# Kernel tuning notes

Measured on AMD Instinct MI355X. Metric: run time of the kernel, lower is better.

## Reference

```python
import jax, jax.numpy as jnp
import numpy as np

N_HEAD = 16
ROPE_BASE = 10000.0
ROPE_SCALE = 1.0

B, T, C = 4, 2048, 1024


def _rope_cos_sin(seq_len, head_dim, dtype):
    inv_freq = 1.0 / (ROPE_BASE ** (jnp.arange(0, head_dim, 2, dtype=jnp.float32) / head_dim))
    t = jnp.arange(seq_len, dtype=jnp.float32) * ROPE_SCALE
    freqs = jnp.einsum('t,d->td', t, inv_freq)          # [T, D/2]
    emb = jnp.concatenate([freqs, freqs], axis=-1)       # [T, D]
    return jnp.cos(emb).astype(dtype), jnp.sin(emb).astype(dtype)


def _rotate_half(x):
    x1, x2 = jnp.split(x, 2, axis=-1)
    return jnp.concatenate([-x2, x1], axis=-1)


def setup_inputs() -> dict:
    key = jax.random.key(0)
    ks = jax.random.split(key, 5)
    s = 1.0 / np.sqrt(C)  # modest init scale to keep logits sane
    return {
        'x': jax.random.normal(ks[0], (B, T, C), dtype=jnp.float32),
        'wq': jax.random.normal(ks[1], (C, C), dtype=jnp.float32) * s,
        'wk': jax.random.normal(ks[2], (C, C), dtype=jnp.float32) * s,
        'wv': jax.random.normal(ks[3], (C, C), dtype=jnp.float32) * s,
        'wp': jax.random.normal(ks[4], (C, C), dtype=jnp.float32) * s,
    }


def reference(x, wq, wk, wv, wp):
    # x: [B, T, C]; weights are torch Linear layout [out, in] -> y = x @ W.T
    Bx, Tx, Cx = x.shape
    H = N_HEAD
    D = Cx // H
    scale = D ** -0.5

    def split_heads(y):  # [B,T,C] -> [B,H,T,D]
        return y.reshape(Bx, Tx, H, D).transpose(0, 2, 1, 3)

    q = split_heads(x @ wq.T)
    k = split_heads(x @ wk.T)
    v = split_heads(x @ wv.T)

    cos, sin = _rope_cos_sin(Tx, D, x.dtype)  # [T, D] each
    cos = cos[None, None, :, :]
    sin = sin[None, None, :, :]
    q = q * cos + _rotate_half(q) * sin
    k = k * cos + _rotate_half(k) * sin

    att = jnp.einsum('bhtd,bhsd->bhts', q, k) * scale  # [B,H,T,T]
    causal = jnp.tril(jnp.ones((Tx, Tx), dtype=bool))
    att = jnp.where(causal[None, None], att, -jnp.inf)
    att = jax.nn.softmax(att, axis=-1)

    y = jnp.einsum('bhts,bhsd->bhtd', att, v)          # [B,H,T,D]
    y = y.transpose(0, 2, 1, 3).reshape(Bx, Tx, Cx)    # [B,T,C]
    return y @ wp.T
```

## Files before the change

### kernel.cpp

```cpp
#include <hip/hip_runtime.h>
#include <hip/hip_bf16.h>

typedef __attribute__((ext_vector_type(8))) short short8;
typedef __attribute__((ext_vector_type(4))) float f32x4;
typedef unsigned short u16;

#define DEV static __device__ __forceinline__

constexpr int Bsz = 4, Tn = 2048, Cn = 1024, Hn = 16, Dn = 64;
constexpr int TP = Tn + 32;
constexpr int VROWS = 80;
#define QSCL 0.1803368801111204f

DEV u16 f2bf(float f) {
    union { float f; unsigned u; } v{f};
    return (u16)((v.u + 0x8000u) >> 16);
}
DEV float bf2f(u16 u) {
    union { unsigned u; float f; } v;
    v.u = ((unsigned)u) << 16;
    return v.f;
}

DEV void gload_lds16(const void* g, void* l) {
    __builtin_amdgcn_global_load_lds((const __attribute__((address_space(1))) void*)g,
                                     (__attribute__((address_space(3))) void*)l, 16, 0, 0);
}

__global__ void cvt_kernel(const float* __restrict__ in, u16* __restrict__ out, int n4) {
    int i = blockIdx.x * blockDim.x + threadIdx.x;
    int stride = gridDim.x * blockDim.x;
    for (; i < n4; i += stride) {
        float4 v = ((const float4*)in)[i];
        short4 o;
        o.x = (short)f2bf(v.x); o.y = (short)f2bf(v.y);
        o.z = (short)f2bf(v.z); o.w = (short)f2bf(v.w);
        ((short4*)out)[i] = o;
    }
}

__global__ void cvtw_kernel(const float* __restrict__ w0, const float* __restrict__ w1,
                            const float* __restrict__ w2, const float* __restrict__ w3,
                            u16* o0, u16* o1, u16* o2, u16* o3) {
    const float* src = blockIdx.y == 0 ? w0 : blockIdx.y == 1 ? w1 : blockIdx.y == 2 ? w2 : w3;
    u16* dst = blockIdx.y == 0 ? o0 : blockIdx.y == 1 ? o1 : blockIdx.y == 2 ? o2 : o3;
    int i = blockIdx.x * blockDim.x + threadIdx.x;
    float4 v = ((const float4*)src)[i];
    short4 o;
    o.x = (short)f2bf(v.x); o.y = (short)f2bf(v.y);
    o.z = (short)f2bf(v.z); o.w = (short)f2bf(v.w);
    ((short4*)dst)[i] = o;
}

__global__ void trig_kernel(float* __restrict__ cs, float* __restrict__ sn) {
    int idx = blockIdx.x * blockDim.x + threadIdx.x;
    int t = idx >> 5, i = idx & 31;
    double inv = pow(10000.0, -(double)i / 32.0);
    double a = (double)t * inv;
    cs[idx] = (float)cos(a);
    sn[idx] = (float)sin(a);
}

__global__ void rope_kernel(u16* __restrict__ q, u16* __restrict__ k,
                            const float* __restrict__ cs, const float* __restrict__ sn) {
    int idx = blockIdx.x * blockDim.x + threadIdx.x;
    const int half = Bsz * Hn * Tn * 32;
    float scl = 1.0f;
    u16* p;
    if (idx >= half) { idx -= half; p = k; }
    else             { p = q; scl = QSCL; }
    int row = idx >> 5, i = idx & 31;
    int t = row & (Tn - 1);
    float c = cs[(t << 5) + i], s = sn[(t << 5) + i];
    u16* pr = p + ((long)row << 6);
    float x1 = bf2f(pr[i]), x2 = bf2f(pr[i + 32]);
    pr[i]      = f2bf((x1 * c - x2 * s) * scl);
    pr[i + 32] = f2bf((x2 * c + x1 * s) * scl);
}

__global__ __launch_bounds__(256, 2) void transpose_v(const u16* __restrict__ in,
                                                      u16* __restrict__ out) {
    __shared__ u16 tile[64][68];
    int bh = blockIdx.y;
    long t0 = (long)blockIdx.x * 64;
    int tid = threadIdx.x;
#pragma unroll
    for (int c = 0; c < 2; c++) {
        int idx = c * 256 + tid;
        int r = idx >> 3, col = (idx & 7) << 3;
        *(short8*)&tile[r][col] = *(const short8*)&in[((long)bh * Tn + t0 + r) * 64 + col];
    }
    __syncthreads();
#pragma unroll
    for (int c = 0; c < 2; c++) {
        int idx = c * 256 + tid;
        int d = idx >> 3, tcol = (idx & 7) << 3;
        short8 v;
#pragma unroll
        for (int j = 0; j < 8; j++) v[j] = tile[tcol + j][d];
        *(short8*)&out[((long)bh * VROWS + d) * TP + t0 + tcol] = v;
    }
}

__global__ void fill_ones(u16* __restrict__ vt) {
    long idx = (long)blockIdx.x * 256 + threadIdx.x;
    long bh = idx / (16 * TP);
    long rem = idx % (16 * TP);
    long r = rem / TP, t = rem % TP;
    vt[(bh * VROWS + 64 + r) * TP + t] = (r == 0) ? (u16)0x3f80 : (u16)0;
}

template <int MODE>
__global__ __launch_bounds__(256, 2) void gemm_bt(
    const u16* __restrict__ A,
    const u16* __restrict__ B0, const u16* __restrict__ B1, const u16* __restrict__ B2,
    void* __restrict__ O0, void* __restrict__ O1, void* __restrict__ O2,
    int M, int N, int K) {
    __shared__ u16 As[128 * 32];
    __shared__ u16 Bs[128 * 32];

    const u16* Bp = B0;
    void* Op = O0;
    if (MODE == 0) {
        if (blockIdx.z == 1) { Bp = B1; Op = O1; }
        else if (blockIdx.z == 2) { Bp = B2; Op = O2; }
    }
    int tid = threadIdx.x;
    int w = tid >> 6, lane = tid & 63;
    int lr = lane & 15, lg = lane >> 4;
    int wr = w >> 1, wc = w & 1;
    long brow = (long)blockIdx.x * 128, bcol = (long)blockIdx.y * 128;

    f32x4 acc[4][4] = {};
    const u16* Arow = A + brow * K;
    const u16* Brow = Bp + bcol * K;

    for (int k0 = 0; k0 < K; k0 += 32) {
        __syncthreads();
#pragma unroll
        for (int c = 0; c < 2; c++) {
            int idx = c * 256 + tid;
            int row = idx >> 2, col = (idx & 3) << 3;
            const u16* ga = Arow + (long)row * K + k0 + col;
            const u16* gb = Brow + (long)row * K + k0 + col;
            char* la = (char*)As + (size_t)(c * 256 + (tid & 192)) * 16;
            char* lb = (char*)Bs + (size_t)(c * 256 + (tid & 192)) * 16;
            gload_lds16(ga, la);
            gload_lds16(gb, lb);
        }
        __syncthreads();
        short8 a[4], b[4];
#pragma unroll
        for (int i = 0; i < 4; i++)
            a[i] = *(const short8*)&As[(64 * wr + 16 * i + lr) * 32 + lg * 8];
#pragma unroll
        for (int j = 0; j < 4; j++)
            b[j] = *(const short8*)&Bs[(64 * wc + 16 * j + lr) * 32 + lg * 8];
#pragma unroll
        for (int i = 0; i < 4; i++)
#pragma unroll
            for (int j = 0; j < 4; j++)
                acc[i][j] = __builtin_amdgcn_mfma_f32_16x16x32_bf16(a[i], b[j], acc[i][j], 0, 0, 0);
    }

#pragma unroll
    for (int i = 0; i < 4; i++)
#pragma unroll
        for (int j = 0; j < 4; j++)
#pragma unroll
            for (int jj = 0; jj < 4; jj++) {
                long gr = brow + 64 * wr + 16 * i + lg * 4 + jj;
                long gc = bcol + 64 * wc + 16 * j + lr;
                float v = acc[i][j][jj];
                if (MODE == 0) {
                    long b_ = gr >> 11, t_ = gr & 2047, h_ = gc >> 6, d_ = gc & 63;
                    ((u16*)Op)[(((b_ * Hn + h_) * Tn + t_) << 6) + d_] = f2bf(v);
                } else {
                    ((float*)Op)[gr * N + gc] = v;
                }
            }
}

__global__ __launch_bounds__(256, 2) void attn_kernel(
    const u16* __restrict__ Q, const u16* __restrict__ K, const u16* __restrict__ VT,
    u16* __restrict__ Yb) {
    __shared__ u16 plds[4][32][68];

    int tid = threadIdx.x;
    int w = tid >> 6, lane = tid & 63;
    int lr = lane & 15, lg = lane >> 4;
    int gid = blockIdx.x;
    int xcd = gid & 7;
    int sl = gid >> 3;
    int bh = ((sl >> 3) << 3) + xcd;
    int pairi = (sl & 7) * 4 + w;

    const u16* Qp = Q + (long)bh * Tn * Dn;
    const u16* Kp = K + (long)bh * Tn * Dn;
    const u16* VTp = VT + (long)bh * VROWS * TP;
    long b_ = bh >> 4, h_ = bh & 15;

#pragma unroll
    for (int pass = 0; pass < 2; pass++) {
        int qt = pass == 0 ? pairi : 63 - pairi;
        int q0 = qt * 32;

        short8 aq[2][2];
#pragma unroll
        for (int qi = 0; qi < 2; qi++)
#pragma unroll
            for (int ks = 0; ks < 2; ks++)
                aq[qi][ks] = *(const short8*)&Qp[(long)(q0 + qi * 16 + lr) * 64 + ks * 32 + lg * 8];

        f32x4 acc[2][5] = {};
        float m_[2][4];
#pragma unroll
        for (int qi = 0; qi < 2; qi++)
#pragma unroll
            for (int jj = 0; jj < 4; jj++) m_[qi][jj] = -1e30f;

        auto iter = [&](auto mc, int kv0) {
            constexpr bool MASKED = decltype(mc)::value;
            short8 bk[4][2];
#pragma unroll
            for (int cblk = 0; cblk < 4; cblk++) {
                const u16* kb = &Kp[(long)(kv0 + cblk * 16 + lr) * 64 + lg * 8];
                bk[cblk][0] = *(const short8*)kb;
                bk[cblk][1] = *(const short8*)(kb + 32);
            }
            short8 bv[2][5];
#pragma unroll
            for (int ks = 0; ks < 2; ks++)
#pragma unroll
                for (int dblk = 0; dblk < 5; dblk++)
                    bv[ks][dblk] = *(const short8*)&VTp[(long)(dblk * 16 + lr) * TP + kv0 + ks * 32 + lg * 8];
            f32x4 s[2][4];
#pragma unroll
            for (int cblk = 0; cblk < 4; cblk++)
#pragma unroll
                for (int qi = 0; qi < 2; qi++) {
                    f32x4 sc = {};
                    sc = __builtin_amdgcn_mfma_f32_16x16x32_bf16(aq[qi][0], bk[cblk][0], sc, 0, 0, 0);
                    sc = __builtin_amdgcn_mfma_f32_16x16x32_bf16(aq[qi][1], bk[cblk][1], sc, 0, 0, 0);
                    if (MASKED) {
                        int col = kv0 + cblk * 16 + lr;
#pragma unroll
                        for (int jj = 0; jj < 4; jj++) {
                            int row = q0 + qi * 16 + lg * 4 + jj;
                            if (col > row) sc[jj] = -1e30f;
                        }
                    }
                    s[qi][cblk] = sc;
                }
            float pm[2][4];
            bool grow = false;
#pragma unroll
            for (int qi = 0; qi < 2; qi++)
#pragma unroll
                for (int jj = 0; jj < 4; jj++) {
                    pm[qi][jj] = fmaxf(fmaxf(s[qi][0][jj], s[qi][1][jj]),
                                       fmaxf(s[qi][2][jj], s[qi][3][jj]));
                    grow = grow || (pm[qi][jj] > m_[qi][jj] + 8.0f);
                }
            if (__any(grow)) {
#pragma unroll
                for (int qi = 0; qi < 2; qi++)
#pragma unroll
                    for (int jj = 0; jj < 4; jj++) {
                        float v = pm[qi][jj];
                        v = fmaxf(v, __shfl_xor(v, 1));
                        v = fmaxf(v, __shfl_xor(v, 2));
                        v = fmaxf(v, __shfl_xor(v, 4));
                        v = fmaxf(v, __shfl_xor(v, 8));
                        float mn = fmaxf(m_[qi][jj], v);
                        float alpha = __builtin_amdgcn_exp2f(m_[qi][jj] - mn);
                        m_[qi][jj] = mn;
#pragma unroll
                        for (int dblk = 0; dblk < 5; dblk++) acc[qi][dblk][jj] *= alpha;
                    }
            }
#pragma unroll
            for (int qi = 0; qi < 2; qi++)
#pragma unroll
                for (int cblk = 0; cblk < 4; cblk++)
#pragma unroll
                    for (int jj = 0; jj < 4; jj++)
                        plds[w][qi * 16 + lg * 4 + jj][cblk * 16 + lr] =
                            f2bf(__builtin_amdgcn_exp2f(s[qi][cblk][jj] - m_[qi][jj]));
            short8 pa[2][2];
#pragma unroll
            for (int qi = 0; qi < 2; qi++)
#pragma unroll
                for (int ks = 0; ks < 2; ks++)
                    pa[qi][ks] = *(const short8*)&plds[w][qi * 16 + lr][ks * 32 + lg * 8];
#pragma unroll
            for (int ks = 0; ks < 2; ks++)
#pragma unroll
                for (int dblk = 0; dblk < 5; dblk++)
#pragma unroll
                    for (int qi = 0; qi < 2; qi++)
                        acc[qi][dblk] = __builtin_amdgcn_mfma_f32_16x16x32_bf16(
                            pa[qi][ks], bv[ks][dblk], acc[qi][dblk], 0, 0, 0);
        };

        int kv_end = q0 + 32;
        int last = ((kv_end - 1) >> 6) << 6;
        for (int kv0 = 0; kv0 < last; kv0 += 64)
            iter(std::integral_constant<bool, false>{}, kv0);
        iter(std::integral_constant<bool, true>{}, last);

#pragma unroll
        for (int qi = 0; qi < 2; qi++)
#pragma unroll
            for (int jj = 0; jj < 4; jj++) {
                float l = __shfl(acc[qi][4][jj], lane & 48);
                float rl = 1.0f / l;
                int row = q0 + qi * 16 + lg * 4 + jj;
#pragma unroll
                for (int dblk = 0; dblk < 4; dblk++) {
                    int d = dblk * 16 + lr;
                    Yb[((b_ * Tn + row) * Cn) + h_ * 64 + d] = f2bf(acc[qi][dblk][jj] * rl);
                }
            }
    }
}

extern "C" void kernel_launch(void* const* d_in, const int* in_sizes, int n_in,
                              void* d_out, int out_size, void* d_ws, size_t ws_size,
                              hipStream_t stream) {
    const float* x  = (const float*)d_in[0];
    const float* wq = (const float*)d_in[1];
    const float* wk = (const float*)d_in[2];
    const float* wv = (const float*)d_in[3];
    const float* wp = (const float*)d_in[4];

    char* ws = (char*)d_ws;
    size_t off = 0;
    auto alloc = [&](size_t bytes) {
        char* p = ws + off;
        off += (bytes + 255) & ~(size_t)255;
        return p;
    };
    const size_t BTC = (size_t)Bsz * Tn * Cn;
    u16* xb  = (u16*)alloc(BTC * 2);
    u16* wqb = (u16*)alloc((size_t)Cn * Cn * 2);
    u16* wkb = (u16*)alloc((size_t)Cn * Cn * 2);
    u16* wvb = (u16*)alloc((size_t)Cn * Cn * 2);
    u16* wpb = (u16*)alloc((size_t)Cn * Cn * 2);
    u16* qr  = (u16*)alloc(BTC * 2);
    u16* kr  = (u16*)alloc(BTC * 2);
    u16* vr  = (u16*)alloc(BTC * 2);
    u16* yb  = (u16*)alloc(BTC * 2);
    float* cs = (float*)alloc((size_t)Tn * 32 * 4);
    float* sn = (float*)alloc((size_t)Tn * 32 * 4);
    u16* vt  = xb;

    int M = Bsz * Tn;
    cvt_kernel<<<1024, 256, 0, stream>>>(x, xb, (int)(BTC / 4));
    cvtw_kernel<<<dim3(Cn * Cn / 4 / 256, 4), 256, 0, stream>>>(
        wq, wk, wv, wp, wqb, wkb, wvb, wpb);
    trig_kernel<<<(Tn * 32) / 256, 256, 0, stream>>>(cs, sn);

    gemm_bt<0><<<dim3(M / 128, Cn / 128, 3), 256, 0, stream>>>(
        xb, wqb, wkb, wvb, qr, kr, vr, M, Cn, Cn);

    int nrows = Bsz * Hn * Tn;
    rope_kernel<<<(2 * nrows * 32) / 256, 256, 0, stream>>>(qr, kr, cs, sn);

    transpose_v<<<dim3(Tn / 64, Bsz * Hn), 256, 0, stream>>>(vr, vt);
    fill_ones<<<(64 * 16 * TP) / 256, 256, 0, stream>>>(vt);

    attn_kernel<<<dim3(512), 256, 0, stream>>>(qr, kr, vt, yb);

    gemm_bt<1><<<dim3(M / 128, Cn / 128, 1), 256, 0, stream>>>(
        yb, wpb, wpb, wpb, d_out, nullptr, nullptr, M, Cn, Cn);
}
```

Before: 233.4 us.

## Fuse RoPE into QK GEMM epilogue, write V transposed, widen attention blocks

The QK projection GEMM now applies rotary embedding and the Q scale in its epilogue, pairing accumulator columns d and d+32, so the separate rope kernel goes away. V is computed as W_v·x^T by a new GEMM mode that writes straight into the transposed, padded VT layout, which removes the transpose kernel and the intermediate V buffer. The attention kernel runs 512-thread blocks where each of 8 waves handles one query tile, replacing the two sequential passes per wave. The fused epilogues use scattered 2-byte stores, and the larger attention blocks may change occupancy.

```diff
diff --git a/kernel.cpp b/kernel.cpp
--- a/kernel.cpp
+++ b/kernel.cpp
@@ -61,47 +61,6 @@
     sn[idx] = (float)sin(a);
 }
 
-__global__ void rope_kernel(u16* __restrict__ q, u16* __restrict__ k,
-                            const float* __restrict__ cs, const float* __restrict__ sn) {
-    int idx = blockIdx.x * blockDim.x + threadIdx.x;
-    const int half = Bsz * Hn * Tn * 32;
-    float scl = 1.0f;
-    u16* p;
-    if (idx >= half) { idx -= half; p = k; }
-    else             { p = q; scl = QSCL; }
-    int row = idx >> 5, i = idx & 31;
-    int t = row & (Tn - 1);
-    float c = cs[(t << 5) + i], s = sn[(t << 5) + i];
-    u16* pr = p + ((long)row << 6);
-    float x1 = bf2f(pr[i]), x2 = bf2f(pr[i + 32]);
-    pr[i]      = f2bf((x1 * c - x2 * s) * scl);
-    pr[i + 32] = f2bf((x2 * c + x1 * s) * scl);
-}
-
-__global__ __launch_bounds__(256, 2) void transpose_v(const u16* __restrict__ in,
-                                                      u16* __restrict__ out) {
-    __shared__ u16 tile[64][68];
-    int bh = blockIdx.y;
-    long t0 = (long)blockIdx.x * 64;
-    int tid = threadIdx.x;
-#pragma unroll
-    for (int c = 0; c < 2; c++) {
-        int idx = c * 256 + tid;
-        int r = idx >> 3, col = (idx & 7) << 3;
-        *(short8*)&tile[r][col] = *(const short8*)&in[((long)bh * Tn + t0 + r) * 64 + col];
-    }
-    __syncthreads();
-#pragma unroll
-    for (int c = 0; c < 2; c++) {
-        int idx = c * 256 + tid;
-        int d = idx >> 3, tcol = (idx & 7) << 3;
-        short8 v;
-#pragma unroll
-        for (int j = 0; j < 8; j++) v[j] = tile[tcol + j][d];
-        *(short8*)&out[((long)bh * VROWS + d) * TP + t0 + tcol] = v;
-    }
-}
-
 __global__ void fill_ones(u16* __restrict__ vt) {
     long idx = (long)blockIdx.x * 256 + threadIdx.x;
     long bh = idx / (16 * TP);
@@ -113,17 +72,19 @@
 template <int MODE>
 __global__ __launch_bounds__(256, 2) void gemm_bt(
     const u16* __restrict__ A,
-    const u16* __restrict__ B0, const u16* __restrict__ B1, const u16* __restrict__ B2,
-    void* __restrict__ O0, void* __restrict__ O1, void* __restrict__ O2,
+    const u16* __restrict__ B0, const u16* __restrict__ B1,
+    void* __restrict__ O0, void* __restrict__ O1,
+    const float* __restrict__ CS, const float* __restrict__ SN,
     int M, int N, int K) {
     __shared__ u16 As[128 * 32];
     __shared__ u16 Bs[128 * 32];
 
     const u16* Bp = B0;
     void* Op = O0;
+    float scl = 1.0f;
     if (MODE == 0) {
         if (blockIdx.z == 1) { Bp = B1; Op = O1; }
-        else if (blockIdx.z == 2) { Bp = B2; Op = O2; }
+        else scl = QSCL;
     }
     int tid = threadIdx.x;
     int w = tid >> 6, lane = tid & 63;
@@ -163,28 +124,52 @@
                 acc[i][j] = __builtin_amdgcn_mfma_f32_16x16x32_bf16(a[i], b[j], acc[i][j], 0, 0, 0);
     }
 
-#pragma unroll
-    for (int i = 0; i < 4; i++)
-#pragma unroll
-        for (int j = 0; j < 4; j++)
+    if (MODE == 0) {
+        u16* Op16 = (u16*)Op;
+#pragma unroll
+        for (int i = 0; i < 4; i++)
 #pragma unroll
             for (int jj = 0; jj < 4; jj++) {
                 long gr = brow + 64 * wr + 16 * i + lg * 4 + jj;
-                long gc = bcol + 64 * wc + 16 * j + lr;
-                float v = acc[i][j][jj];
-                if (MODE == 0) {
-                    long b_ = gr >> 11, t_ = gr & 2047, h_ = gc >> 6, d_ = gc & 63;
-                    ((u16*)Op)[(((b_ * Hn + h_) * Tn + t_) << 6) + d_] = f2bf(v);
-                } else {
-                    ((float*)Op)[gr * N + gc] = v;
+                long b_ = gr >> 11, t_ = gr & 2047;
+#pragma unroll
+                for (int j = 0; j < 2; j++) {
+                    int di = 16 * j + lr;
+                    float c = CS[(t_ << 5) + di], s = SN[(t_ << 5) + di];
+                    float x1 = acc[i][j][jj], x2 = acc[i][j + 2][jj];
+                    float o1 = (x1 * c - x2 * s) * scl;
+                    float o2 = (x2 * c + x1 * s) * scl;
+                    long gc = bcol + 64 * wc + 16 * j + lr;
+                    long h_ = gc >> 6;
+                    long base = (((b_ * Hn + h_) * Tn + t_) << 6) + (gc & 63);
+                    Op16[base] = f2bf(o1);
+                    Op16[base + 32] = f2bf(o2);
                 }
             }
-}
-
-__global__ __launch_bounds__(256, 2) void attn_kernel(
+    } else {
+#pragma unroll
+        for (int i = 0; i < 4; i++)
+#pragma unroll
+            for (int j = 0; j < 4; j++)
+#pragma unroll
+                for (int jj = 0; jj < 4; jj++) {
+                    long gr = brow + 64 * wr + 16 * i + lg * 4 + jj;
+                    long gc = bcol + 64 * wc + 16 * j + lr;
+                    float v = acc[i][j][jj];
+                    if (MODE == 1) {
+                        ((float*)Op)[gr * N + gc] = v;
+                    } else {
+                        long h_ = gr >> 6, d_ = gr & 63, b_ = gc >> 11, t_ = gc & 2047;
+                        ((u16*)Op)[((b_ * Hn + h_) * VROWS + d_) * TP + t_] = f2bf(v);
+                    }
+                }
+    }
+}
+
+__global__ __launch_bounds__(512, 4) void attn_kernel(
     const u16* __restrict__ Q, const u16* __restrict__ K, const u16* __restrict__ VT,
     u16* __restrict__ Yb) {
-    __shared__ u16 plds[4][32][68];
+    __shared__ u16 plds[8][32][68];
 
     int tid = threadIdx.x;
     int w = tid >> 6, lane = tid & 63;
@@ -193,136 +178,132 @@
     int xcd = gid & 7;
     int sl = gid >> 3;
     int bh = ((sl >> 3) << 3) + xcd;
-    int pairi = (sl & 7) * 4 + w;
+    int slot = sl & 7;
+    int qt = (w < 4) ? slot * 4 + w : 63 - (slot * 4 + (w - 4));
+    int q0 = qt * 32;
 
     const u16* Qp = Q + (long)bh * Tn * Dn;
     const u16* Kp = K + (long)bh * Tn * Dn;
     const u16* VTp = VT + (long)bh * VROWS * TP;
     long b_ = bh >> 4, h_ = bh & 15;
 
-#pragma unroll
-    for (int pass = 0; pass < 2; pass++) {
-        int qt = pass == 0 ? pairi : 63 - pairi;
-        int q0 = qt * 32;
-
-        short8 aq[2][2];
+    short8 aq[2][2];
+#pragma unroll
+    for (int qi = 0; qi < 2; qi++)
+#pragma unroll
+        for (int ks = 0; ks < 2; ks++)
+            aq[qi][ks] = *(const short8*)&Qp[(long)(q0 + qi * 16 + lr) * 64 + ks * 32 + lg * 8];
+
+    f32x4 acc[2][5] = {};
+    float m_[2][4];
+#pragma unroll
+    for (int qi = 0; qi < 2; qi++)
+#pragma unroll
+        for (int jj = 0; jj < 4; jj++) m_[qi][jj] = -1e30f;
+
+    auto iter = [&](auto mc, int kv0) {
+        constexpr bool MASKED = decltype(mc)::value;
+        short8 bk[4][2];
+#pragma unroll
+        for (int cblk = 0; cblk < 4; cblk++) {
+            const u16* kb = &Kp[(long)(kv0 + cblk * 16 + lr) * 64 + lg * 8];
+            bk[cblk][0] = *(const short8*)kb;
+            bk[cblk][1] = *(const short8*)(kb + 32);
+        }
+        short8 bv[2][5];
+#pragma unroll
+        for (int ks = 0; ks < 2; ks++)
+#pragma unroll
+            for (int dblk = 0; dblk < 5; dblk++)
+                bv[ks][dblk] = *(const short8*)&VTp[(long)(dblk * 16 + lr) * TP + kv0 + ks * 32 + lg * 8];
+        f32x4 s[2][4];
+#pragma unroll
+        for (int cblk = 0; cblk < 4; cblk++)
+#pragma unroll
+            for (int qi = 0; qi < 2; qi++) {
+                f32x4 sc = {};
+                sc = __builtin_amdgcn_mfma_f32_16x16x32_bf16(aq[qi][0], bk[cblk][0], sc, 0, 0, 0);
+                sc = __builtin_amdgcn_mfma_f32_16x16x32_bf16(aq[qi][1], bk[cblk][1], sc, 0, 0, 0);
+                if (MASKED) {
+                    int col = kv0 + cblk * 16 + lr;
+#pragma unroll
+                    for (int jj = 0; jj < 4; jj++) {
+                        int row = q0 + qi * 16 + lg * 4 + jj;
+                        if (col > row) sc[jj] = -1e30f;
+                    }
+                }
+                s[qi][cblk] = sc;
+            }
+        float pm[2][4];
+        bool grow = false;
 #pragma unroll
         for (int qi = 0; qi < 2; qi++)
 #pragma unroll
+            for (int jj = 0; jj < 4; jj++) {
+                pm[qi][jj] = fmaxf(fmaxf(s[qi][0][jj], s[qi][1][jj]),
+                                   fmaxf(s[qi][2][jj], s[qi][3][jj]));
+                grow = grow || (pm[qi][jj] > m_[qi][jj] + 8.0f);
+            }
+        if (__any(grow)) {
+#pragma unroll
+            for (int qi = 0; qi < 2; qi++)
+#pragma unroll
+                for (int jj = 0; jj < 4; jj++) {
+                    float v = pm[qi][jj];
+                    v = fmaxf(v, __shfl_xor(v, 1));
+                    v = fmaxf(v, __shfl_xor(v, 2));
+                    v = fmaxf(v, __shfl_xor(v, 4));
+                    v = fmaxf(v, __shfl_xor(v, 8));
+                    float mn = fmaxf(m_[qi][jj], v);
+                    float alpha = __builtin_amdgcn_exp2f(m_[qi][jj] - mn);
+                    m_[qi][jj] = mn;
+#pragma unroll
+                    for (int dblk = 0; dblk < 5; dblk++) acc[qi][dblk][jj] *= alpha;
+                }
+        }
+#pragma unroll
+        for (int qi = 0; qi < 2; qi++)
+#pragma unroll
+            for (int cblk = 0; cblk < 4; cblk++)
+#pragma unroll
+                for (int jj = 0; jj < 4; jj++)
+                    plds[w][qi * 16 + lg * 4 + jj][cblk * 16 + lr] =
+                        f2bf(__builtin_amdgcn_exp2f(s[qi][cblk][jj] - m_[qi][jj]));
+        short8 pa[2][2];
+#pragma unroll
+        for (int qi = 0; qi < 2; qi++)
+#pragma unroll
             for (int ks = 0; ks < 2; ks++)
-                aq[qi][ks] = *(const short8*)&Qp[(long)(q0 + qi * 16 + lr) * 64 + ks * 32 + lg * 8];
-
-        f32x4 acc[2][5] = {};
-        float m_[2][4];
-#pragma unroll
-        for (int qi = 0; qi < 2; qi++)
-#pragma unroll
-            for (int jj = 0; jj < 4; jj++) m_[qi][jj] = -1e30f;
-
-        auto iter = [&](auto mc, int kv0) {
-            constexpr bool MASKED = decltype(mc)::value;
-            short8 bk[4][2];
-#pragma unroll
-            for (int cblk = 0; cblk < 4; cblk++) {
-                const u16* kb = &Kp[(long)(kv0 + cblk * 16 + lr) * 64 + lg * 8];
-                bk[cblk][0] = *(const short8*)kb;
-                bk[cblk][1] = *(const short8*)(kb + 32);
+                pa[qi][ks] = *(const short8*)&plds[w][qi * 16 + lr][ks * 32 + lg * 8];
+#pragma unroll
+        for (int ks = 0; ks < 2; ks++)
+#pragma unroll
+            for (int dblk = 0; dblk < 5; dblk++)
+#pragma unroll
+                for (int qi = 0; qi < 2; qi++)
+                    acc[qi][dblk] = __builtin_amdgcn_mfma_f32_16x16x32_bf16(
+                        pa[qi][ks], bv[ks][dblk], acc[qi][dblk], 0, 0, 0);
+    };
+
+    int kv_end = q0 + 32;
+    int last = ((kv_end - 1) >> 6) << 6;
+    for (int kv0 = 0; kv0 < last; kv0 += 64)
+        iter(std::integral_constant<bool, false>{}, kv0);
+    iter(std::integral_constant<bool, true>{}, last);
+
+#pragma unroll
+    for (int qi = 0; qi < 2; qi++)
+#pragma unroll
+        for (int jj = 0; jj < 4; jj++) {
+            float l = __shfl(acc[qi][4][jj], lane & 48);
+            float rl = 1.0f / l;
+            int row = q0 + qi * 16 + lg * 4 + jj;
+#pragma unroll
+            for (int dblk = 0; dblk < 4; dblk++) {
+                int d = dblk * 16 + lr;
+                Yb[((b_ * Tn + row) * Cn) + h_ * 64 + d] = f2bf(acc[qi][dblk][jj] * rl);
             }
-            short8 bv[2][5];
-#pragma unroll
-            for (int ks = 0; ks < 2; ks++)
-#pragma unroll
-                for (int dblk = 0; dblk < 5; dblk++)
-                    bv[ks][dblk] = *(const short8*)&VTp[(long)(dblk * 16 + lr) * TP + kv0 + ks * 32 + lg * 8];
-            f32x4 s[2][4];
-#pragma unroll
-            for (int cblk = 0; cblk < 4; cblk++)
-#pragma unroll
-                for (int qi = 0; qi < 2; qi++) {
-                    f32x4 sc = {};
-                    sc = __builtin_amdgcn_mfma_f32_16x16x32_bf16(aq[qi][0], bk[cblk][0], sc, 0, 0, 0);
-                    sc = __builtin_amdgcn_mfma_f32_16x16x32_bf16(aq[qi][1], bk[cblk][1], sc, 0, 0, 0);
-                    if (MASKED) {
-                        int col = kv0 + cblk * 16 + lr;
-#pragma unroll
-                        for (int jj = 0; jj < 4; jj++) {
-                            int row = q0 + qi * 16 + lg * 4 + jj;
-                            if (col > row) sc[jj] = -1e30f;
-                        }
-                    }
-                    s[qi][cblk] = sc;
-                }
-            float pm[2][4];
-            bool grow = false;
-#pragma unroll
-            for (int qi = 0; qi < 2; qi++)
-#pragma unroll
-                for (int jj = 0; jj < 4; jj++) {
-                    pm[qi][jj] = fmaxf(fmaxf(s[qi][0][jj], s[qi][1][jj]),
-                                       fmaxf(s[qi][2][jj], s[qi][3][jj]));
-                    grow = grow || (pm[qi][jj] > m_[qi][jj] + 8.0f);
-                }
-            if (__any(grow)) {
-#pragma unroll
-                for (int qi = 0; qi < 2; qi++)
-#pragma unroll
-                    for (int jj = 0; jj < 4; jj++) {
-                        float v = pm[qi][jj];
-                        v = fmaxf(v, __shfl_xor(v, 1));
-                        v = fmaxf(v, __shfl_xor(v, 2));
-                        v = fmaxf(v, __shfl_xor(v, 4));
-                        v = fmaxf(v, __shfl_xor(v, 8));
-                        float mn = fmaxf(m_[qi][jj], v);
-                        float alpha = __builtin_amdgcn_exp2f(m_[qi][jj] - mn);
-                        m_[qi][jj] = mn;
-#pragma unroll
-                        for (int dblk = 0; dblk < 5; dblk++) acc[qi][dblk][jj] *= alpha;
-                    }
-            }
-#pragma unroll
-            for (int qi = 0; qi < 2; qi++)
-#pragma unroll
-                for (int cblk = 0; cblk < 4; cblk++)
-#pragma unroll
-                    for (int jj = 0; jj < 4; jj++)
-                        plds[w][qi * 16 + lg * 4 + jj][cblk * 16 + lr] =
-                            f2bf(__builtin_amdgcn_exp2f(s[qi][cblk][jj] - m_[qi][jj]));
-            short8 pa[2][2];
-#pragma unroll
-            for (int qi = 0; qi < 2; qi++)
-#pragma unroll
-                for (int ks = 0; ks < 2; ks++)
-                    pa[qi][ks] = *(const short8*)&plds[w][qi * 16 + lr][ks * 32 + lg * 8];
-#pragma unroll
-            for (int ks = 0; ks < 2; ks++)
-#pragma unroll
-                for (int dblk = 0; dblk < 5; dblk++)
-#pragma unroll
-                    for (int qi = 0; qi < 2; qi++)
-                        acc[qi][dblk] = __builtin_amdgcn_mfma_f32_16x16x32_bf16(
-                            pa[qi][ks], bv[ks][dblk], acc[qi][dblk], 0, 0, 0);
-        };
-
-        int kv_end = q0 + 32;
-        int last = ((kv_end - 1) >> 6) << 6;
-        for (int kv0 = 0; kv0 < last; kv0 += 64)
-            iter(std::integral_constant<bool, false>{}, kv0);
-        iter(std::integral_constant<bool, true>{}, last);
-
-#pragma unroll
-        for (int qi = 0; qi < 2; qi++)
-#pragma unroll
-            for (int jj = 0; jj < 4; jj++) {
-                float l = __shfl(acc[qi][4][jj], lane & 48);
-                float rl = 1.0f / l;
-                int row = q0 + qi * 16 + lg * 4 + jj;
-#pragma unroll
-                for (int dblk = 0; dblk < 4; dblk++) {
-                    int d = dblk * 16 + lr;
-                    Yb[((b_ * Tn + row) * Cn) + h_ * 64 + d] = f2bf(acc[qi][dblk][jj] * rl);
-                }
-            }
-    }
+        }
 }
 
 extern "C" void kernel_launch(void* const* d_in, const int* in_sizes, int n_in,
@@ -349,11 +330,10 @@
     u16* wpb = (u16*)alloc((size_t)Cn * Cn * 2);
     u16* qr  = (u16*)alloc(BTC * 2);
     u16* kr  = (u16*)alloc(BTC * 2);
-    u16* vr  = (u16*)alloc(BTC * 2);
-    u16* yb  = (u16*)alloc(BTC * 2);
+    u16* vt  = (u16*)alloc((size_t)64 * VROWS * TP * 2);
     float* cs = (float*)alloc((size_t)Tn * 32 * 4);
     float* sn = (float*)alloc((size_t)Tn * 32 * 4);
-    u16* vt  = xb;
+    u16* yb  = xb;
 
     int M = Bsz * Tn;
     cvt_kernel<<<1024, 256, 0, stream>>>(x, xb, (int)(BTC / 4));
@@ -361,17 +341,15 @@
         wq, wk, wv, wp, wqb, wkb, wvb, wpb);
     trig_kernel<<<(Tn * 32) / 256, 256, 0, stream>>>(cs, sn);
 
-    gemm_bt<0><<<dim3(M / 128, Cn / 128, 3), 256, 0, stream>>>(
-        xb, wqb, wkb, wvb, qr, kr, vr, M, Cn, Cn);
-
-    int nrows = Bsz * Hn * Tn;
-    rope_kernel<<<(2 * nrows * 32) / 256, 256, 0, stream>>>(qr, kr, cs, sn);
-
-    transpose_v<<<dim3(Tn / 64, Bsz * Hn), 256, 0, stream>>>(vr, vt);
+    gemm_bt<0><<<dim3(M / 128, Cn / 128, 2), 256, 0, stream>>>(
+        xb, wqb, wkb, qr, kr, cs, sn, M, Cn, Cn);
+
+    gemm_bt<2><<<dim3(Cn / 128, M / 128), 256, 0, stream>>>(
+        wvb, xb, nullptr, vt, nullptr, nullptr, nullptr, Cn, M, Cn);
     fill_ones<<<(64 * 16 * TP) / 256, 256, 0, stream>>>(vt);
 
-    attn_kernel<<<dim3(512), 256, 0, stream>>>(qr, kr, vt, yb);
-
-    gemm_bt<1><<<dim3(M / 128, Cn / 128, 1), 256, 0, stream>>>(
-        yb, wpb, wpb, wpb, d_out, nullptr, nullptr, M, Cn, Cn);
-}
+    attn_kernel<<<dim3(512), 512, 0, stream>>>(qr, kr, vt, yb);
+
+    gemm_bt<1><<<dim3(M / 128, Cn / 128), 256, 0, stream>>>(
+        yb, wpb, nullptr, d_out, nullptr, nullptr, nullptr, M, Cn, Cn);
+}
```

New measurement: 365.6 us. +56.6%, slower.
